# Performance work log

Hardware: AMD Instinct MI355X
Metric: run time of the kernel (lower is better)

## Reference

```python
import jax, jax.numpy as jnp
import numpy as np

N_HEADS_Q = 16
GKV = 4
EPS = 1e-6


def setup_inputs() -> dict:
    key = jax.random.key(0)
    ks = jax.random.split(key, 5)
    B, Tq, Tk, D, d = 2, 2048, 2048, 2048, 128
    return {
        "x_q": jax.random.normal(ks[0], (B, Tq, D), dtype=jnp.float32),
        "k_ctx": jax.random.normal(ks[1], (B, Tk, GKV, d), dtype=jnp.float32),
        "v_ctx": jax.random.normal(ks[2], (B, Tk, GKV, d), dtype=jnp.float32),
        "w_q": jax.random.normal(ks[3], (D, D), dtype=jnp.float32) * (1.0 / np.sqrt(D)),
        "w_out": jax.random.normal(ks[4], (D, D), dtype=jnp.float32) * (1.0 / np.sqrt(D)),
        "norm_w": jnp.ones((D,), dtype=jnp.float32),
    }


def reference(x_q, k_ctx, v_ctx, w_q, w_out, norm_w):
    B, Tq, D = x_q.shape
    _, Tk, G, d = k_ctx.shape
    H = N_HEADS_Q
    r = H // G  # query heads per KV group (repeat_interleave factor)

    # RMSNorm on queries
    xn = x_q * jax.lax.rsqrt(jnp.mean(jnp.square(x_q), axis=-1, keepdims=True) + EPS) * norm_w
    # q projection (torch Linear: y = x @ W^T), split heads grouped as (G, r)
    q = jnp.einsum('btd,od->bto', xn, w_q).reshape(B, Tq, G, r, d)

    # GQA attention: head h = g*r + i attends with KV group g (same math as
    # repeat_interleave of K/V along the head dim, without materializing it)
    scale = 1.0 / np.sqrt(d)
    scores = jnp.einsum('bqgrd,bkgd->bgrqk', q, k_ctx) * scale  # (B,G,r,Tq,Tk)
    probs = jax.nn.softmax(scores, axis=-1)
    ctx = jnp.einsum('bgrqk,bkgd->bqgrd', probs, v_ctx).reshape(B, Tq, D)

    return jnp.einsum('btd,od->bto', ctx, w_out)
```

## Files before the change

kernel.cpp:

```cpp
#include <hip/hip_runtime.h>
#include <stdint.h>

typedef unsigned short u16;
typedef __attribute__((ext_vector_type(4))) float f32x4;
typedef __attribute__((ext_vector_type(8))) __bf16 bf16x8;

#define AS1(p) ((const __attribute__((address_space(1))) unsigned int*)(p))
#define AS3(p) ((__attribute__((address_space(3))) unsigned int*)(p))
#define GL2LDS16(g, l) __builtin_amdgcn_global_load_lds(AS1(g), AS3(l), 16, 0, 0)

__device__ __forceinline__ u16 f2bf(float x) {
  union { float f; uint32_t u; } v; v.f = x;
  return (u16)((v.u + 0x7fffu + ((v.u >> 16) & 1u)) >> 16);
}
__device__ __forceinline__ uint32_t pkbf(float a, float b) {
  union { __bf16 h[2]; uint32_t u; } x;
  x.h[0] = (__bf16)a; x.h[1] = (__bf16)b;
  return x.u;
}
__device__ __forceinline__ void store_c(u16* p, float v) { *p = f2bf(v); }
__device__ __forceinline__ void store_c(float* p, float v) { *p = v; }

__global__ __launch_bounds__(256) void cvt_kernel(const float* __restrict__ in,
                                                  u16* __restrict__ out, int n4) {
  const int stride = gridDim.x * blockDim.x;
  for (int i = blockIdx.x * blockDim.x + threadIdx.x; i < n4; i += stride) {
    const float4 v = ((const float4*)in)[i];
    ushort4 o;
    o.x = f2bf(v.x); o.y = f2bf(v.y); o.z = f2bf(v.z); o.w = f2bf(v.w);
    ((ushort4*)out)[i] = o;
  }
}

__global__ __launch_bounds__(256) void rmsnorm_kernel(const float* __restrict__ x,
                                                      const float* __restrict__ w,
                                                      u16* __restrict__ out) {
  const int row = blockIdx.x;
  const int tid = threadIdx.x;
  const float* xr = x + (size_t)row * 2048;
  const float4 a0 = ((const float4*)xr)[tid];
  const float4 a1 = ((const float4*)xr)[tid + 256];
  float ss = a0.x*a0.x + a0.y*a0.y + a0.z*a0.z + a0.w*a0.w
           + a1.x*a1.x + a1.y*a1.y + a1.z*a1.z + a1.w*a1.w;
#pragma unroll
  for (int m = 1; m < 64; m <<= 1) ss += __shfl_xor(ss, m);
  __shared__ float red[4];
  if ((tid & 63) == 0) red[tid >> 6] = ss;
  __syncthreads();
  const float tot = red[0] + red[1] + red[2] + red[3];
  const float sc = rsqrtf(tot * (1.0f / 2048.0f) + 1e-6f);
  const float4 w0 = ((const float4*)w)[tid];
  const float4 w1 = ((const float4*)w)[tid + 256];
  u16* orow = out + (size_t)row * 2048;
  ushort4 o0, o1;
  o0.x = f2bf(a0.x * sc * w0.x); o0.y = f2bf(a0.y * sc * w0.y);
  o0.z = f2bf(a0.z * sc * w0.z); o0.w = f2bf(a0.w * sc * w0.w);
  o1.x = f2bf(a1.x * sc * w1.x); o1.y = f2bf(a1.y * sc * w1.y);
  o1.z = f2bf(a1.z * sc * w1.z); o1.w = f2bf(a1.w * sc * w1.w);
  ((ushort4*)orow)[tid] = o0;
  ((ushort4*)orow)[tid + 256] = o1;
}

template<typename OutT>
__global__ __launch_bounds__(256) void gemm_bt(const u16* __restrict__ A,
                                               const u16* __restrict__ Bm,
                                               OutT* __restrict__ C,
                                               int M, int N, int K, float scale) {
  __shared__ __align__(16) u16 As[128 * 32];
  __shared__ __align__(16) u16 Bs[128 * 32];
  const int tid = threadIdx.x;
  const int lane = tid & 63;
  const int w = tid >> 6, wm = w >> 1, wn = w & 1;
  const int m0 = blockIdx.y * 128, n0 = blockIdx.x * 128;
  f32x4 acc[4][4] = {};
  for (int kt = 0; kt < K; kt += 32) {
    __syncthreads();
#pragma unroll
    for (int j = 0; j < 2; ++j) {
      const int c = j * 256 + tid;
      const int row = c >> 2, ch = c & 3;
      GL2LDS16(A + (size_t)(m0 + row) * K + kt + ch * 8, As + (size_t)c * 8);
      GL2LDS16(Bm + (size_t)(n0 + row) * K + kt + ch * 8, Bs + (size_t)c * 8);
    }
    __syncthreads();
    bf16x8 af[4], bfr[4];
#pragma unroll
    for (int i = 0; i < 4; ++i) {
      af[i]  = *(const bf16x8*)(As + (wm * 64 + i * 16 + (lane & 15)) * 32 + (lane >> 4) * 8);
      bfr[i] = *(const bf16x8*)(Bs + (wn * 64 + i * 16 + (lane & 15)) * 32 + (lane >> 4) * 8);
    }
#pragma unroll
    for (int mi = 0; mi < 4; ++mi)
#pragma unroll
      for (int ni = 0; ni < 4; ++ni)
        acc[mi][ni] = __builtin_amdgcn_mfma_f32_16x16x32_bf16(af[mi], bfr[ni], acc[mi][ni], 0, 0, 0);
  }
#pragma unroll
  for (int mi = 0; mi < 4; ++mi)
#pragma unroll
    for (int r = 0; r < 4; ++r) {
      const int row = m0 + wm * 64 + mi * 16 + (lane >> 4) * 4 + r;
#pragma unroll
      for (int ni = 0; ni < 4; ++ni) {
        const int col = n0 + wn * 64 + ni * 16 + (lane & 15);
        store_c(C + (size_t)row * N + col, acc[mi][ni][r] * scale);
      }
    }
}

__global__ __launch_bounds__(256) void attn_kernel(const u16* __restrict__ q,
                                                   const u16* __restrict__ kbf,
                                                   const u16* __restrict__ vbf,
                                                   u16* __restrict__ ctx) {
  __shared__ __align__(16) char smem[81920];
  u16* const Qs  = (u16*)smem;
  u16* const Ks  = (u16*)smem;
  u16* const VTb = (u16*)(smem + 32768);
  const int tid = threadIdx.x;
  const int lane = tid & 63;
  const int w = tid >> 6;
  const int l15 = lane & 15, lhi = lane >> 4;
  const int sxor = (l15 & 7) << 3;
  u16* const PsW = (u16*)(smem + 65536) + w * 2048;
  const int qt = blockIdx.x;
  const int bh = blockIdx.y;
  const int b = bh >> 4, h = bh & 15, g = h >> 2;
  const size_t qbase  = ((size_t)(b * 2048 + qt * 128)) * 2048 + h * 128;
  const size_t kvbase = (size_t)b * 1048576 + g * 128;

#pragma unroll
  for (int j = 0; j < 8; ++j) {
    const int c = j * 256 + tid;
    const int row = c >> 4;
    const int dim0 = ((c & 15) ^ (row & 7)) << 3;
    GL2LDS16(q + qbase + (size_t)row * 2048 + dim0, Qs + (size_t)c * 8);
  }
  __syncthreads();
  bf16x8 qf[2][4];
#pragma unroll
  for (int qs = 0; qs < 2; ++qs) {
    const int qrow = w * 32 + qs * 16 + l15;
#pragma unroll
    for (int dk = 0; dk < 4; ++dk) {
      const int el = qrow * 128 + ((dk * 32 + lhi * 8) ^ ((qrow & 7) << 3));
      qf[qs][dk] = *(const bf16x8*)(Qs + el);
    }
  }
  __syncthreads();

  uint4 vv[4];
  auto stageK = [&](int buf, int kt0) {
    u16* Kb = Ks + buf * 8192;
#pragma unroll
    for (int j = 0; j < 4; ++j) {
      const int c = j * 256 + tid;
      const int key = c >> 4;
      const int dim0 = ((c & 15) ^ (key & 7)) << 3;
      GL2LDS16(kbf + kvbase + (size_t)(kt0 + key) * 512 + dim0, Kb + (size_t)c * 8);
    }
  };
  auto loadV = [&](int kt0) {
#pragma unroll
    for (int j = 0; j < 4; ++j) {
      const int c = j * 256 + tid;
      const int key = c & 63;
      const int dim0 = (c >> 6) << 3;
      vv[j] = *(const uint4*)(vbf + kvbase + (size_t)(kt0 + key) * 512 + dim0);
    }
  };
  auto writeV = [&](int buf) {
    u16* Vb = VTb + buf * 8192;
#pragma unroll
    for (int j = 0; j < 4; ++j) {
      const int c = j * 256 + tid;
      const int key = c & 63;
      const int dim0 = (c >> 6) << 3;
      const uint32_t* pv = (const uint32_t*)&vv[j];
#pragma unroll
      for (int i = 0; i < 4; ++i) {
        Vb[(dim0 + 2 * i)     * 64 + (key ^ ((2 * i)     << 3))] = (u16)(pv[i] & 0xffff);
        Vb[(dim0 + 2 * i + 1) * 64 + (key ^ ((2 * i + 1) << 3))] = (u16)(pv[i] >> 16);
      }
    }
  };

  stageK(0, 0);
  loadV(0);
  writeV(0);
  __syncthreads();

  f32x4 cacc[8][2] = {};
  float mrow[2], lrow[2];
#pragma unroll
  for (int qs = 0; qs < 2; ++qs) { mrow[qs] = -3.0e38f; lrow[qs] = 0.f; }

  int cur = 0;
  for (int kt0 = 0; kt0 < 2048; kt0 += 64) {
    const int nxt = cur ^ 1;
    const bool pref = (kt0 + 64) < 2048;
    if (pref) { stageK(nxt, kt0 + 64); loadV(kt0 + 64); }

    const u16* Kb = Ks + cur * 8192;
    f32x4 st[4][2] = {};
#pragma unroll
    for (int dk = 0; dk < 4; ++dk) {
      bf16x8 kf[4];
#pragma unroll
      for (int ni = 0; ni < 4; ++ni) {
        const int key = ni * 16 + l15;
        const int el = key * 128 + ((dk * 32 + lhi * 8) ^ ((key & 7) << 3));
        kf[ni] = *(const bf16x8*)(Kb + el);
      }
      __builtin_amdgcn_s_setprio(1);
#pragma unroll
      for (int ni = 0; ni < 4; ++ni)
#pragma unroll
        for (int qs = 0; qs < 2; ++qs)
          st[ni][qs] = __builtin_amdgcn_mfma_f32_16x16x32_bf16(kf[ni], qf[qs][dk], st[ni][qs], 0, 0, 0);
      __builtin_amdgcn_s_setprio(0);
    }

#pragma unroll
    for (int qs = 0; qs < 2; ++qs) {
      float pm = -3.0e38f;
#pragma unroll
      for (int ni = 0; ni < 4; ++ni)
#pragma unroll
        for (int r = 0; r < 4; ++r) pm = fmaxf(pm, st[ni][qs][r]);
      pm = fmaxf(pm, __shfl_xor(pm, 16));
      pm = fmaxf(pm, __shfl_xor(pm, 32));
      if (!__all(pm <= mrow[qs] + 8.0f)) {
        const float mnew = fmaxf(mrow[qs], pm);
        const float f = exp2f(mrow[qs] - mnew);
        mrow[qs] = mnew;
        lrow[qs] *= f;
#pragma unroll
        for (int nd = 0; nd < 8; ++nd) cacc[nd][qs] *= f;
      }
      float ps = 0.f;
#pragma unroll
      for (int ni = 0; ni < 4; ++ni) {
        const float a0 = exp2f(st[ni][qs][0] - mrow[qs]);
        const float a1 = exp2f(st[ni][qs][1] - mrow[qs]);
        const float a2 = exp2f(st[ni][qs][2] - mrow[qs]);
        const float a3 = exp2f(st[ni][qs][3] - mrow[qs]);
        ps += (a0 + a1) + (a2 + a3);
        uint2 val; val.x = pkbf(a0, a1); val.y = pkbf(a2, a3);
        *(uint2*)(PsW + (qs * 16 + l15) * 64 + ((ni * 16 + lhi * 4) ^ sxor)) = val;
      }
      ps += __shfl_xor(ps, 16);
      ps += __shfl_xor(ps, 32);
      lrow[qs] += ps;
    }

    const u16* Vb = VTb + cur * 8192;
    __builtin_amdgcn_s_setprio(1);
#pragma unroll
    for (int ks = 0; ks < 2; ++ks) {
      bf16x8 pf[2];
#pragma unroll
      for (int qs = 0; qs < 2; ++qs)
        pf[qs] = *(const bf16x8*)(PsW + (qs * 16 + l15) * 64 + ((ks * 32 + lhi * 8) ^ sxor));
#pragma unroll
      for (int nd = 0; nd < 8; ++nd) {
        const bf16x8 vf = *(const bf16x8*)(Vb + (nd * 16 + l15) * 64 + ((ks * 32 + lhi * 8) ^ sxor));
#pragma unroll
        for (int qs = 0; qs < 2; ++qs)
          cacc[nd][qs] = __builtin_amdgcn_mfma_f32_16x16x32_bf16(vf, pf[qs], cacc[nd][qs], 0, 0, 0);
      }
    }
    __builtin_amdgcn_s_setprio(0);

    if (pref) writeV(nxt);
    __syncthreads();
    cur = nxt;
  }

  const int qrow_base = b * 2048 + qt * 128 + w * 32;
#pragma unroll
  for (int qs = 0; qs < 2; ++qs) {
    const float inv = 1.0f / lrow[qs];
    const int row = qrow_base + qs * 16 + l15;
    u16* orow = ctx + (size_t)row * 2048 + h * 128 + lhi * 4;
#pragma unroll
    for (int nd = 0; nd < 8; ++nd) {
      uint2 val;
      val.x = pkbf(cacc[nd][qs][0] * inv, cacc[nd][qs][1] * inv);
      val.y = pkbf(cacc[nd][qs][2] * inv, cacc[nd][qs][3] * inv);
      *(uint2*)(orow + nd * 16) = val;
    }
  }
}

extern "C" void kernel_launch(void* const* d_in, const int* in_sizes, int n_in,
                              void* d_out, int out_size, void* d_ws, size_t ws_size,
                              hipStream_t stream) {
  const float* x_q    = (const float*)d_in[0];
  const float* k_ctx  = (const float*)d_in[1];
  const float* v_ctx  = (const float*)d_in[2];
  const float* w_q    = (const float*)d_in[3];
  const float* w_out  = (const float*)d_in[4];
  const float* norm_w = (const float*)d_in[5];
  float* out = (float*)d_out;

  char* ws = (char*)d_ws;
  u16* wq_bf = (u16*)(ws);
  u16* wo_bf = (u16*)(ws + 8388608);
  u16* k_bf  = (u16*)(ws + 16777216);
  u16* v_bf  = (u16*)(ws + 20971520);
  u16* xn    = (u16*)(ws + 25165824);
  u16* qb    = (u16*)(ws + 41943040);
  u16* ctxb  = xn;

  const float kscale = 0.08838834764831845f * 1.4426950408889634f;

  cvt_kernel<<<1024, 256, 0, stream>>>(w_q,   wq_bf, 4194304 / 4);
  cvt_kernel<<<1024, 256, 0, stream>>>(w_out, wo_bf, 4194304 / 4);
  cvt_kernel<<<512,  256, 0, stream>>>(k_ctx, k_bf,  2097152 / 4);
  cvt_kernel<<<512,  256, 0, stream>>>(v_ctx, v_bf,  2097152 / 4);
  rmsnorm_kernel<<<4096, 256, 0, stream>>>(x_q, norm_w, xn);
  gemm_bt<u16><<<dim3(16, 32), 256, 0, stream>>>(xn, wq_bf, qb, 4096, 2048, 2048, kscale);
  attn_kernel<<<dim3(16, 32), 256, 0, stream>>>(qb, k_bf, v_bf, ctxb);
  gemm_bt<float><<<dim3(16, 32), 256, 0, stream>>>(ctxb, wo_bf, out, 4096, 2048, 2048, 1.0f);
}
```

Before: 405.4 us.

## Pre-transpose V to bf16 globally and stage it via direct global-to-LDS loads

A new kernel converts V to bf16 and writes it transposed to (b,g,d,t) layout. The attention kernel then stages V tiles with async global_load_lds, replacing the register load plus scattered 2-byte LDS transpose writes done every iteration. Three of the separate conversion launches are merged into one. The cost is an extra transpose pass through LDS in preprocessing, and a per-row swizzle is now applied when reading V fragments.

```diff
diff --git a/kernel.cpp b/kernel.cpp
--- a/kernel.cpp
+++ b/kernel.cpp
@@ -21,44 +21,55 @@
 __device__ __forceinline__ void store_c(u16* p, float v) { *p = f2bf(v); }
 __device__ __forceinline__ void store_c(float* p, float v) { *p = v; }
 
-__global__ __launch_bounds__(256) void cvt_kernel(const float* __restrict__ in,
-                                                  u16* __restrict__ out, int n4) {
+__global__ __launch_bounds__(256) void cvt3_kernel(const float* __restrict__ a,
+                                                   const float* __restrict__ bb,
+                                                   const float* __restrict__ c,
+                                                   u16* __restrict__ oa,
+                                                   u16* __restrict__ ob,
+                                                   u16* __restrict__ oc) {
   const int stride = gridDim.x * blockDim.x;
-  for (int i = blockIdx.x * blockDim.x + threadIdx.x; i < n4; i += stride) {
-    const float4 v = ((const float4*)in)[i];
+  for (int i = blockIdx.x * blockDim.x + threadIdx.x; i < 2621440; i += stride) {
+    const float* src; u16* dst; int idx;
+    if (i < 1048576)      { src = a;  dst = oa; idx = i; }
+    else if (i < 2097152) { src = bb; dst = ob; idx = i - 1048576; }
+    else                  { src = c;  dst = oc; idx = i - 2097152; }
+    const float4 v = ((const float4*)src)[idx];
     ushort4 o;
     o.x = f2bf(v.x); o.y = f2bf(v.y); o.z = f2bf(v.z); o.w = f2bf(v.w);
-    ((ushort4*)out)[i] = o;
-  }
-}
-
-__global__ __launch_bounds__(256) void rmsnorm_kernel(const float* __restrict__ x,
-                                                      const float* __restrict__ w,
-                                                      u16* __restrict__ out) {
-  const int row = blockIdx.x;
+    ((ushort4*)dst)[idx] = o;
+  }
+}
+
+__global__ __launch_bounds__(256) void vtrans_kernel(const float* __restrict__ v,
+                                                     u16* __restrict__ vt) {
+  __shared__ u16 tile[64][65];
   const int tid = threadIdx.x;
-  const float* xr = x + (size_t)row * 2048;
-  const float4 a0 = ((const float4*)xr)[tid];
-  const float4 a1 = ((const float4*)xr)[tid + 256];
-  float ss = a0.x*a0.x + a0.y*a0.y + a0.z*a0.z + a0.w*a0.w
-           + a1.x*a1.x + a1.y*a1.y + a1.z*a1.z + a1.w*a1.w;
-#pragma unroll
-  for (int m = 1; m < 64; m <<= 1) ss += __shfl_xor(ss, m);
-  __shared__ float red[4];
-  if ((tid & 63) == 0) red[tid >> 6] = ss;
-  __syncthreads();
-  const float tot = red[0] + red[1] + red[2] + red[3];
-  const float sc = rsqrtf(tot * (1.0f / 2048.0f) + 1e-6f);
-  const float4 w0 = ((const float4*)w)[tid];
-  const float4 w1 = ((const float4*)w)[tid + 256];
-  u16* orow = out + (size_t)row * 2048;
-  ushort4 o0, o1;
-  o0.x = f2bf(a0.x * sc * w0.x); o0.y = f2bf(a0.y * sc * w0.y);
-  o0.z = f2bf(a0.z * sc * w0.z); o0.w = f2bf(a0.w * sc * w0.w);
-  o1.x = f2bf(a1.x * sc * w1.x); o1.y = f2bf(a1.y * sc * w1.y);
-  o1.z = f2bf(a1.z * sc * w1.z); o1.w = f2bf(a1.w * sc * w1.w);
-  ((ushort4*)orow)[tid] = o0;
-  ((ushort4*)orow)[tid + 256] = o1;
+  const int t0 = blockIdx.x * 64;
+  const int bg = blockIdx.y;
+  const int b = bg >> 2, g = bg & 3;
+  const int d0 = blockIdx.z * 64;
+#pragma unroll
+  for (int it = 0; it < 4; ++it) {
+    const int i = (tid >> 4) + it * 16;
+    const int j = (tid & 15) * 4;
+    const float4 x = *(const float4*)(v + (((size_t)(b * 2048 + t0 + i) * 4 + g) * 128 + d0 + j));
+    tile[i][j + 0] = f2bf(x.x);
+    tile[i][j + 1] = f2bf(x.y);
+    tile[i][j + 2] = f2bf(x.z);
+    tile[i][j + 3] = f2bf(x.w);
+  }
+  __syncthreads();
+  const int dd = tid >> 2;
+#pragma unroll
+  for (int it = 0; it < 4; ++it) {
+    const int tt = (tid & 3) * 16 + it * 4;
+    ushort4 o;
+    o.x = tile[tt + 0][dd];
+    o.y = tile[tt + 1][dd];
+    o.z = tile[tt + 2][dd];
+    o.w = tile[tt + 3][dd];
+    *(ushort4*)(vt + (((size_t)bg * 128 + d0 + dd) * 2048 + t0 + tt)) = o;
+  }
 }
 
 template<typename OutT>
@@ -108,9 +119,38 @@
     }
 }
 
+__global__ __launch_bounds__(256) void rmsnorm_kernel(const float* __restrict__ x,
+                                                      const float* __restrict__ w,
+                                                      u16* __restrict__ out) {
+  const int row = blockIdx.x;
+  const int tid = threadIdx.x;
+  const float* xr = x + (size_t)row * 2048;
+  const float4 a0 = ((const float4*)xr)[tid];
+  const float4 a1 = ((const float4*)xr)[tid + 256];
+  float ss = a0.x*a0.x + a0.y*a0.y + a0.z*a0.z + a0.w*a0.w
+           + a1.x*a1.x + a1.y*a1.y + a1.z*a1.z + a1.w*a1.w;
+#pragma unroll
+  for (int m = 1; m < 64; m <<= 1) ss += __shfl_xor(ss, m);
+  __shared__ float red[4];
+  if ((tid & 63) == 0) red[tid >> 6] = ss;
+  __syncthreads();
+  const float tot = red[0] + red[1] + red[2] + red[3];
+  const float sc = rsqrtf(tot * (1.0f / 2048.0f) + 1e-6f);
+  const float4 w0 = ((const float4*)w)[tid];
+  const float4 w1 = ((const float4*)w)[tid + 256];
+  u16* orow = out + (size_t)row * 2048;
+  ushort4 o0, o1;
+  o0.x = f2bf(a0.x * sc * w0.x); o0.y = f2bf(a0.y * sc * w0.y);
+  o0.z = f2bf(a0.z * sc * w0.z); o0.w = f2bf(a0.w * sc * w0.w);
+  o1.x = f2bf(a1.x * sc * w1.x); o1.y = f2bf(a1.y * sc * w1.y);
+  o1.z = f2bf(a1.z * sc * w1.z); o1.w = f2bf(a1.w * sc * w1.w);
+  ((ushort4*)orow)[tid] = o0;
+  ((ushort4*)orow)[tid + 256] = o1;
+}
+
 __global__ __launch_bounds__(256) void attn_kernel(const u16* __restrict__ q,
                                                    const u16* __restrict__ kbf,
-                                                   const u16* __restrict__ vbf,
+                                                   const u16* __restrict__ vt,
                                                    u16* __restrict__ ctx) {
   __shared__ __align__(16) char smem[81920];
   u16* const Qs  = (u16*)smem;
@@ -126,7 +166,8 @@
   const int bh = blockIdx.y;
   const int b = bh >> 4, h = bh & 15, g = h >> 2;
   const size_t qbase  = ((size_t)(b * 2048 + qt * 128)) * 2048 + h * 128;
-  const size_t kvbase = (size_t)b * 1048576 + g * 128;
+  const size_t kbase  = (size_t)b * 1048576 + g * 128;
+  const size_t vtbase = (size_t)(b * 4 + g) * 262144;
 
 #pragma unroll
   for (int j = 0; j < 8; ++j) {
@@ -148,7 +189,6 @@
   }
   __syncthreads();
 
-  uint4 vv[4];
   auto stageK = [&](int buf, int kt0) {
     u16* Kb = Ks + buf * 8192;
 #pragma unroll
@@ -156,37 +196,22 @@
       const int c = j * 256 + tid;
       const int key = c >> 4;
       const int dim0 = ((c & 15) ^ (key & 7)) << 3;
-      GL2LDS16(kbf + kvbase + (size_t)(kt0 + key) * 512 + dim0, Kb + (size_t)c * 8);
+      GL2LDS16(kbf + kbase + (size_t)(kt0 + key) * 512 + dim0, Kb + (size_t)c * 8);
     }
   };
-  auto loadV = [&](int kt0) {
+  auto stageV = [&](int buf, int kt0) {
+    u16* Vb = VTb + buf * 8192;
 #pragma unroll
     for (int j = 0; j < 4; ++j) {
       const int c = j * 256 + tid;
-      const int key = c & 63;
-      const int dim0 = (c >> 6) << 3;
-      vv[j] = *(const uint4*)(vbf + kvbase + (size_t)(kt0 + key) * 512 + dim0);
+      const int d = c >> 3;
+      const int col0 = ((c & 7) ^ (d & 7)) << 3;
+      GL2LDS16(vt + vtbase + (size_t)d * 2048 + kt0 + col0, Vb + (size_t)c * 8);
     }
   };
-  auto writeV = [&](int buf) {
-    u16* Vb = VTb + buf * 8192;
-#pragma unroll
-    for (int j = 0; j < 4; ++j) {
-      const int c = j * 256 + tid;
-      const int key = c & 63;
-      const int dim0 = (c >> 6) << 3;
-      const uint32_t* pv = (const uint32_t*)&vv[j];
-#pragma unroll
-      for (int i = 0; i < 4; ++i) {
-        Vb[(dim0 + 2 * i)     * 64 + (key ^ ((2 * i)     << 3))] = (u16)(pv[i] & 0xffff);
-        Vb[(dim0 + 2 * i + 1) * 64 + (key ^ ((2 * i + 1) << 3))] = (u16)(pv[i] >> 16);
-      }
-    }
-  };
 
   stageK(0, 0);
-  loadV(0);
-  writeV(0);
+  stageV(0, 0);
   __syncthreads();
 
   f32x4 cacc[8][2] = {};
@@ -198,7 +223,7 @@
   for (int kt0 = 0; kt0 < 2048; kt0 += 64) {
     const int nxt = cur ^ 1;
     const bool pref = (kt0 + 64) < 2048;
-    if (pref) { stageK(nxt, kt0 + 64); loadV(kt0 + 64); }
+    if (pref) { stageK(nxt, kt0 + 64); stageV(nxt, kt0 + 64); }
 
     const u16* Kb = Ks + cur * 8192;
     f32x4 st[4][2] = {};
@@ -263,7 +288,8 @@
         pf[qs] = *(const bf16x8*)(PsW + (qs * 16 + l15) * 64 + ((ks * 32 + lhi * 8) ^ sxor));
 #pragma unroll
       for (int nd = 0; nd < 8; ++nd) {
-        const bf16x8 vf = *(const bf16x8*)(Vb + (nd * 16 + l15) * 64 + ((ks * 32 + lhi * 8) ^ sxor));
+        const int row = nd * 16 + l15;
+        const bf16x8 vf = *(const bf16x8*)(Vb + row * 64 + ((ks * 32 + lhi * 8) ^ ((row & 7) << 3)));
 #pragma unroll
         for (int qs = 0; qs < 2; ++qs)
           cacc[nd][qs] = __builtin_amdgcn_mfma_f32_16x16x32_bf16(vf, pf[qs], cacc[nd][qs], 0, 0, 0);
@@ -271,7 +297,6 @@
     }
     __builtin_amdgcn_s_setprio(0);
 
-    if (pref) writeV(nxt);
     __syncthreads();
     cur = nxt;
   }
@@ -307,19 +332,17 @@
   u16* wq_bf = (u16*)(ws);
   u16* wo_bf = (u16*)(ws + 8388608);
   u16* k_bf  = (u16*)(ws + 16777216);
-  u16* v_bf  = (u16*)(ws + 20971520);
+  u16* v_t   = (u16*)(ws + 20971520);
   u16* xn    = (u16*)(ws + 25165824);
   u16* qb    = (u16*)(ws + 41943040);
   u16* ctxb  = xn;
 
   const float kscale = 0.08838834764831845f * 1.4426950408889634f;
 
-  cvt_kernel<<<1024, 256, 0, stream>>>(w_q,   wq_bf, 4194304 / 4);
-  cvt_kernel<<<1024, 256, 0, stream>>>(w_out, wo_bf, 4194304 / 4);
-  cvt_kernel<<<512,  256, 0, stream>>>(k_ctx, k_bf,  2097152 / 4);
-  cvt_kernel<<<512,  256, 0, stream>>>(v_ctx, v_bf,  2097152 / 4);
+  cvt3_kernel<<<2048, 256, 0, stream>>>(w_q, w_out, k_ctx, wq_bf, wo_bf, k_bf);
+  vtrans_kernel<<<dim3(32, 8, 2), 256, 0, stream>>>(v_ctx, v_t);
   rmsnorm_kernel<<<4096, 256, 0, stream>>>(x_q, norm_w, xn);
   gemm_bt<u16><<<dim3(16, 32), 256, 0, stream>>>(xn, wq_bf, qb, 4096, 2048, 2048, kscale);
-  attn_kernel<<<dim3(16, 32), 256, 0, stream>>>(qb, k_bf, v_bf, ctxb);
+  attn_kernel<<<dim3(16, 32), 256, 0, stream>>>(qb, k_bf, v_t, ctxb);
   gemm_bt<float><<<dim3(16, 32), 256, 0, stream>>>(ctxb, wo_bf, out, 4096, 2048, 2048, 1.0f);
 }
```

After: 390.7 us. 3.6% less time.
